# Optimization experiments

Measured on AMD Instinct MI355X. Metric: run time of the kernel, lower is better.

## Reference

```python
import jax, jax.numpy as jnp
import numpy as np
from jax import lax

H = 256  # hidden_dim
NDIM = 3
K = 32   # k_neighbors


def sincos_embed(coords, dim, ndim):
    # ContinuousSinCosEmbed: per-coordinate sin/cos features, zero-padded to `dim`.
    dpn = dim // ndim          # channels per coordinate
    half = dpn // 2
    freqs = 1.0 / (10000.0 ** (jnp.arange(half, dtype=coords.dtype) / half))
    ang = coords[..., :, None] * freqs                      # (..., ndim, half)
    emb = jnp.concatenate([jnp.sin(ang), jnp.cos(ang)], -1)  # (..., ndim, 2*half)
    emb = emb.reshape(coords.shape[:-1] + (ndim * 2 * half,))
    pad = dim - ndim * 2 * half
    if pad:
        emb = jnp.concatenate([emb, jnp.zeros(emb.shape[:-1] + (pad,), emb.dtype)], -1)
    return emb


def setup_inputs() -> dict:
    key = jax.random.key(0)
    ks = jax.random.split(key, 8)
    N, S = 50000, 1024
    positions = jax.random.uniform(ks[0], (N, NDIM), dtype=jnp.float32) * 10.0
    supernode_indices = jax.random.randint(ks[1], (S,), 0, N, dtype=jnp.int32)
    g = 1.0 / np.sqrt(H)
    W1 = jax.random.normal(ks[2], (H, H), jnp.float32) * g
    b1 = jnp.zeros((H,), jnp.float32)
    W2 = jax.random.normal(ks[3], (H, H), jnp.float32) * g
    b2 = jnp.zeros((H,), jnp.float32)
    Wp = jax.random.normal(ks[4], (2 * H, H), jnp.float32) * (1.0 / np.sqrt(2 * H))
    bp = jnp.zeros((H,), jnp.float32)
    return {"positions": positions, "supernode_indices": supernode_indices,
            "W1": W1, "b1": b1, "W2": W2, "b2": b2, "Wp": Wp, "bp": bp}


def reference(positions, supernode_indices, W1, b1, W2, b2, Wp, bp):
    # positions: (N, 3); supernode_indices: (S,)
    sup_pos = positions[supernode_indices]                 # (S, 3)
    # kNN neighbor search via dense pairwise squared distances (memory-bound)
    diff = sup_pos[:, None, :] - positions[None, :, :]     # (S, N, 3)
    dist2 = jnp.sum(diff * diff, axis=-1)                  # (S, N)
    _, nbr_idx = lax.top_k(-dist2, K)                      # (S, K)
    nbr_pos = positions[nbr_idx]                           # (S, K, 3)
    # relpos mode: embed (relative position, distance) -> ndim+1 = 4 coords
    rel = sup_pos[:, None, :] - nbr_pos                    # (S, K, 3)
    d = jnp.sqrt(jnp.sum(rel * rel, axis=-1, keepdims=True))  # (S, K, 1)
    rel_feat = jnp.concatenate([rel, d], axis=-1)          # (S, K, 4)
    msg_in = sincos_embed(rel_feat, H, NDIM + 1)           # (S, K, H)
    # message MLP: Dense -> gelu -> Dense
    h = jax.nn.gelu(jnp.einsum('ski,ij->skj', msg_in, W1) + b1)
    msgs = jnp.einsum('ski,ij->skj', h, W2) + b2           # (S, K, H)
    # scatter-reduce: mean over neighbors per supernode
    agg = jnp.mean(msgs, axis=1)                           # (S, H)
    # supernode absolute position embedding, concat, project
    sup_emb = sincos_embed(sup_pos, H, NDIM)               # (S, H)
    feats = jnp.concatenate([sup_emb, agg], axis=-1)       # (S, 2H)
    out = feats @ Wp + bp                                  # (S, H)
    return out[None]                                        # (1, S, H)
```

## Files before the change

kernel.cpp:

```cpp
#include <hip/hip_runtime.h>
#include <hip/hip_bf16.h>
#include <math.h>

typedef short bf16x8 __attribute__((ext_vector_type(8)));
typedef float f32x4  __attribute__((ext_vector_type(4)));

constexpr int   H     = 256;
constexpr int   KNB   = 32;
constexpr int   TPB   = 512;
constexpr int   GC    = 16;
constexpr float HINV  = 1.6f;
constexpr float HCEL  = 0.625f;
constexpr int   SLOTS = 32;
constexpr int   OCAP  = 256;
constexpr int   CAP   = 512;

__device__ __forceinline__ ushort f2bf(float x) {
    unsigned u = __float_as_uint(x);
    u += 0x7FFF + ((u >> 16) & 1);
    return (ushort)(u >> 16);
}

__device__ __forceinline__ float gelu_fast(float x) {
    float u = 0.7978845608028654f * (x + 0.044715f * x * x * x);
    float t = exp2f(-2.885390081777927f * u);
    return x / (1.0f + t);
}

__device__ __forceinline__ int cell_of(float x, float y, float z) {
    int cx = min(GC - 1, max(0, (int)(x * HINV)));
    int cy = min(GC - 1, max(0, (int)(y * HINV)));
    int cz = min(GC - 1, max(0, (int)(z * HINV)));
    return (cz * GC + cy) * GC + cx;
}

__global__ __launch_bounds__(256)
void prep(const float* __restrict__ W1, const float* __restrict__ Wp,
          const float* __restrict__ W2, const float* __restrict__ pos, int N,
          ushort* __restrict__ W1t, ushort* __restrict__ Wpt,
          ushort* __restrict__ W2t, float4* __restrict__ pos4s,
          int* __restrict__ origidx, int* __restrict__ cellcnt,
          int* __restrict__ ovfidx, float4* __restrict__ ovfpos) {
    const int b = blockIdx.x;
    if (b < 64) {
        __shared__ float tile[32][33];
        const int ti = b >> 3, tj = b & 7;
        const int r  = threadIdx.x >> 5, c = threadIdx.x & 31;
#pragma unroll
        for (int rr = r; rr < 32; rr += 8)
            tile[rr][c] = W1[(ti * 32 + rr) * H + tj * 32 + c];
        __syncthreads();
#pragma unroll
        for (int rr = r; rr < 32; rr += 8)
            W1t[(tj * 32 + rr) * H + ti * 32 + c] = f2bf(tile[c][rr]);
    } else if (b < 192) {
        __shared__ float tile[32][33];
        const int b2 = b - 64;
        const int ti = b2 >> 3, tj = b2 & 7;
        const int r  = threadIdx.x >> 5, c = threadIdx.x & 31;
#pragma unroll
        for (int rr = r; rr < 32; rr += 8)
            tile[rr][c] = Wp[(ti * 32 + rr) * H + tj * 32 + c];
        __syncthreads();
#pragma unroll
        for (int rr = r; rr < 32; rr += 8)
            Wpt[(tj * 32 + rr) * (2 * H) + ti * 32 + c] = f2bf(tile[c][rr]);
    } else if (b < 256) {
        __shared__ float tile[32][33];
        const int b2 = b - 192;
        const int ti = b2 >> 3, tj = b2 & 7;
        const int r  = threadIdx.x >> 5, c = threadIdx.x & 31;
#pragma unroll
        for (int rr = r; rr < 32; rr += 8)
            tile[rr][c] = W2[(ti * 32 + rr) * H + tj * 32 + c];
        __syncthreads();
#pragma unroll
        for (int rr = r; rr < 32; rr += 8)
            W2t[(tj * 32 + rr) * H + ti * 32 + c] = f2bf(tile[c][rr]);
    } else {
        const int sb = b - 256;
        const int base = sb * 1024;
        const int t = threadIdx.x;
        auto scat = [&](float x, float y, float z, int i) {
            float4 P = make_float4(x, y, z, 0.f);
            int c = cell_of(x, y, z);
            int slot = atomicAdd(&cellcnt[c], 1);
            if (slot < SLOTS) {
                pos4s[c * SLOTS + slot] = P;
                origidx[c * SLOTS + slot] = i;
            } else {
                int o = atomicAdd(&cellcnt[4096], 1);
                if (o < OCAP) { ovfpos[o] = P; ovfidx[o] = i; }
            }
        };
        if (base + 1024 <= N) {
            const float4* p4 = (const float4*)(pos + (size_t)base * 3);
            float4 f0 = p4[3 * t + 0];
            float4 f1 = p4[3 * t + 1];
            float4 f2 = p4[3 * t + 2];
            const int ib = base + 4 * t;
            scat(f0.x, f0.y, f0.z, ib + 0);
            scat(f0.w, f1.x, f1.y, ib + 1);
            scat(f1.z, f1.w, f2.x, ib + 2);
            scat(f2.y, f2.z, f2.w, ib + 3);
        } else {
            for (int i = base + t; i < N; i += 256)
                scat(pos[3 * i], pos[3 * i + 1], pos[3 * i + 2], i);
        }
    }
}

__global__ __launch_bounds__(TPB, 8)
void fused_knn_mlp(const float* __restrict__ pos,
                   const float4* __restrict__ pos4s,
                   const int* __restrict__ origidx,
                   const int* __restrict__ cellcnt,
                   const int* __restrict__ ovfidx, const float4* __restrict__ ovfpos,
                   const int* __restrict__ supidx,
                   const ushort* __restrict__ W1t, const float* __restrict__ b1,
                   ushort* __restrict__ supEB, ushort* __restrict__ hbB)
{
    __shared__ __align__(16) char pool[16384];
    float* amaxd = (float*)pool;
    int*   acnt  = (int*)(pool + 512);
    int*   ccell = (int*)(pool + 1024);
    int*   ccnt  = (int*)(pool + 2048);
    float* cmnd  = (float*)(pool + 3072);
    int*   cpre  = (int*)(pool + 4096);
    float* d2buf = (float*)(pool + 5120);
    int*   obuf  = (int*)(pool + 7168);
    float* pxb   = (float*)(pool + 9216);
    float* pyb   = (float*)(pool + 11264);
    float* pzb   = (float*)(pool + 13312);
    ushort* msg  = (ushort*)pool;

    __shared__ float rf[KNB][5];
    __shared__ int   selo[KNB];
    __shared__ int   wsum[4];
    __shared__ float tau2_sh, tau32_sh;
    __shared__ int   cnt_sh, ncl;

    const int s    = blockIdx.x;
    const int t    = threadIdx.x;
    const int lane = t & 63;
    const int w    = t >> 6;

    const int sidx = supidx[s];
    const float sx = pos[3 * sidx], sy = pos[3 * sidx + 1], sz = pos[3 * sidx + 2];

    constexpr float L2_10000 = 13.287712379549449f;

    if (t == 0) { ncl = 0; tau2_sh = 301.f; }

    const int scx = min(GC - 1, max(0, (int)(sx * HINV)));
    const int scy = min(GC - 1, max(0, (int)(sy * HINV)));
    const int scz = min(GC - 1, max(0, (int)(sz * HINV)));
    const int ax0 = max(0, scx - 2), ax1 = min(GC - 1, scx + 2);
    const int ay0 = max(0, scy - 2), ay1 = min(GC - 1, scy + 2);
    const int az0 = max(0, scz - 2), az1 = min(GC - 1, scz + 2);
    const int anx = ax1 - ax0 + 1, any_ = ay1 - ay0 + 1, anz = az1 - az0 + 1;
    const int an  = anx * any_ * anz;
    if (t < an) {
        int ci = t;
        int X = ax0 + ci % anx, rem = ci / anx;
        int Y = ay0 + rem % any_, Z = az0 + rem / any_;
        int cell = (Z * GC + Y) * GC + X;
        acnt[ci] = min(cellcnt[cell], SLOTS);
        float lx = X * HCEL, ly = Y * HCEL, lz = Z * HCEL;
        float mx = fmaxf(fabsf(sx - lx), fabsf(lx + HCEL - sx));
        float my = fmaxf(fabsf(sy - ly), fabsf(ly + HCEL - sy));
        float mz = fmaxf(fabsf(sz - lz), fabsf(lz + HCEL - sz));
        amaxd[ci] = mx * mx + my * my + mz * mz;
    }

    if (t < 256) {
        float se = 0.f;
        if (t < 252) {
            int c  = t / 84;
            int rr = t - c * 84;
            int f  = (rr < 42) ? rr : rr - 42;
            float coord = (c == 0) ? sx : ((c == 1) ? sy : sz);
            float ang = coord * exp2f(-(float)f * (L2_10000 / 42.f));
            se = (rr < 42) ? __sinf(ang) : __cosf(ang);
        }
        supEB[s * H + t] = f2bf(se);
    }
    __syncthreads();
    if (t < an) {
        int ci = t;
        float myv = amaxd[ci];
        int Sc = 0;
        for (int j = 0; j < an; j++) {
            bool less = (amaxd[j] < myv) || (amaxd[j] == myv && j < ci);
            Sc += less ? acnt[j] : 0;
        }
        if (Sc < KNB && KNB <= Sc + acnt[ci]) tau2_sh = myv;
    }
    __syncthreads();
    const float tau2 = tau2_sh;
    const float R2 = tau2 + 1e-3f;
    const float R  = sqrtf(R2);
    if (t == 0) tau32_sh = R2;

    const int bx0 = max(0, (int)floorf((sx - R) * HINV));
    const int bx1 = min(GC - 1, (int)floorf((sx + R) * HINV));
    const int by0 = max(0, (int)floorf((sy - R) * HINV));
    const int by1 = min(GC - 1, (int)floorf((sy + R) * HINV));
    const int bz0 = max(0, (int)floorf((sz - R) * HINV));
    const int bz1 = min(GC - 1, (int)floorf((sz + R) * HINV));
    const bool inwin = (bx0 >= ax0 && bx1 <= ax1 && by0 >= ay0 && by1 <= ay1 &&
                        bz0 >= az0 && bz1 <= az1);
    if (inwin) {
        if (t < an) {
            int ci = t;
            int cn = acnt[ci];
            if (cn > 0) {
                int X = ax0 + ci % anx, rem = ci / anx;
                int Y = ay0 + rem % any_, Z = az0 + rem / any_;
                float lx = X * HCEL, ly = Y * HCEL, lz = Z * HCEL;
                float ddx = fmaxf(fmaxf(lx - sx, sx - (lx + HCEL)), 0.f);
                float ddy = fmaxf(fmaxf(ly - sy, sy - (ly + HCEL)), 0.f);
                float ddz = fmaxf(fmaxf(lz - sz, sz - (lz + HCEL)), 0.f);
                float mnd = ddx * ddx + ddy * ddy + ddz * ddz;
                if (mnd <= R2) {
                    int p1 = (amaxd[ci] <= tau2) ? 1 : 0;
                    int cell = (Z * GC + Y) * GC + X;
                    int sl = atomicAdd(&ncl, 1);
                    if (sl < 256) { ccell[sl] = cell; ccnt[sl] = cn | (p1 << 8); cmnd[sl] = mnd; }
                }
            }
        }
    } else {
        const int nbx = bx1 - bx0 + 1, nby = by1 - by0 + 1, nbz = bz1 - bz0 + 1;
        const int ncb = nbx * nby * nbz;
        for (int ci = t; ci < ncb; ci += TPB) {
            int X = bx0 + ci % nbx, rem = ci / nbx;
            int Y = by0 + rem % nby, Z = bz0 + rem / nby;
            float lx = X * HCEL, ly = Y * HCEL, lz = Z * HCEL;
            float ddx = fmaxf(fmaxf(lx - sx, sx - (lx + HCEL)), 0.f);
            float ddy = fmaxf(fmaxf(ly - sy, sy - (ly + HCEL)), 0.f);
            float ddz = fmaxf(fmaxf(lz - sz, sz - (lz + HCEL)), 0.f);
            float mnd = ddx * ddx + ddy * ddy + ddz * ddz;
            if (mnd > R2) continue;
            int cell = (Z * GC + Y) * GC + X;
            int cn = min(cellcnt[cell], SLOTS);
            if (cn == 0) continue;
            float mx = fmaxf(fabsf(sx - lx), fabsf(lx + HCEL - sx));
            float my = fmaxf(fabsf(sy - ly), fabsf(ly + HCEL - sy));
            float mz = fmaxf(fabsf(sz - lz), fabsf(lz + HCEL - sz));
            float amx = mx * mx + my * my + mz * mz;
            int p1 = (amx <= tau2) ? 1 : 0;
            int sl = atomicAdd(&ncl, 1);
            if (sl < 256) { ccell[sl] = cell; ccnt[sl] = cn | (p1 << 8); cmnd[sl] = mnd; }
        }
    }
    __syncthreads();
    const int nclc = min(ncl, 256);

    auto build_prefix = [&](int phase, float tlim) -> int {
        int v = 0;
        if (t < 256) {
            if (t < nclc) {
                int cc = ccnt[t];
                int cn = cc & 0xff;
                int p1 = cc >> 8;
                v = (phase == 1) ? (p1 ? cn : 0)
                                 : ((!p1 && cmnd[t] <= tlim) ? cn : 0);
            }
#pragma unroll
            for (int off = 1; off < 64; off <<= 1) {
                int x = __shfl_up(v, off);
                if (lane >= off) v += x;
            }
            if (lane == 63) wsum[w] = v;
        }
        __syncthreads();
        if (t < 256) {
            int add = 0;
#pragma unroll
            for (int j = 0; j < 4; j++) if (j < w) add += wsum[j];
            cpre[t] = v + add;
        }
        __syncthreads();
        return cpre[255];
    };
    auto bsearch = [&](int j) -> int {
        int lo = 0;
#pragma unroll
        for (int st = 128; st; st >>= 1) {
            int nlo = lo + st;
            if (nlo <= 256 && cpre[nlo - 1] <= j) lo = nlo;
        }
        return lo;
    };

    const int tot1 = build_prefix(1, 0.f);
    const int M1 = min(tot1, CAP);
    if (t < M1) {
        int j = t;
        int lo = bsearch(j);
        int off = j - (lo ? cpre[lo - 1] : 0);
        int u = ccell[lo] * SLOTS + off;
        float4 P = pos4s[u];
        float dx = sx - P.x, dy = sy - P.y, dz = sz - P.z;
        d2buf[j] = dx * dx + dy * dy + dz * dz;
        obuf[j]  = origidx[u];
        pxb[j] = P.x; pyb[j] = P.y; pzb[j] = P.z;
    }
    const int Mp1 = (M1 + 3) & ~3;
    if (M1 + t < Mp1) { d2buf[M1 + t] = INFINITY; obuf[M1 + t] = 0x7fffffff; }
    if (t == 0) cnt_sh = M1;
    __syncthreads();

    if (t < M1) {
        int u = t;
        float myv = d2buf[u];
        int   myo = obuf[u];
        int rank = 0;
        for (int v2 = 0; v2 < Mp1; v2 += 4) {
            float4 dv = *(const float4*)&d2buf[v2];
            int4   iv = *(const int4*)&obuf[v2];
            rank += (dv.x < myv) || (dv.x == myv && iv.x < myo);
            rank += (dv.y < myv) || (dv.y == myv && iv.y < myo);
            rank += (dv.z < myv) || (dv.z == myv && iv.z < myo);
            rank += (dv.w < myv) || (dv.w == myv && iv.w < myo);
        }
        if (rank == KNB - 1) tau32_sh = myv;
    }
    __syncthreads();
    const float tau32 = tau32_sh;

    const int tot2 = build_prefix(2, tau32);
    for (int j0 = 0; j0 < tot2; j0 += TPB) {
        int j = j0 + t;
        bool pass = false; float pd2 = 0.f; int po = 0; float qx = 0, qy = 0, qz = 0;
        if (j < tot2) {
            int lo = bsearch(j);
            int off = j - (lo ? cpre[lo - 1] : 0);
            int u = ccell[lo] * SLOTS + off;
            float4 P = pos4s[u];
            float dx = sx - P.x, dy = sy - P.y, dz = sz - P.z;
            pd2 = dx * dx + dy * dy + dz * dz;
            if (pd2 <= tau32) { pass = true; po = origidx[u]; qx = P.x; qy = P.y; qz = P.z; }
        }
        unsigned long long m = __ballot(pass);
        if (m) {
            int ldr = __ffsll(m) - 1;
            int base = 0;
            if (lane == ldr) base = atomicAdd(&cnt_sh, __popcll(m));
            base = __shfl(base, ldr);
            if (pass) {
                int slp = base + __popcll(m & ((1ull << lane) - 1ull));
                if (slp < CAP) {
                    d2buf[slp] = pd2; obuf[slp] = po;
                    pxb[slp] = qx; pyb[slp] = qy; pzb[slp] = qz;
                }
            }
        }
    }
    {
        int no = min(cellcnt[4096], OCAP);
        for (int j = t; j < no; j += TPB) {
            float4 P = ovfpos[j];
            float dx = sx - P.x, dy = sy - P.y, dz = sz - P.z;
            float pd2 = dx * dx + dy * dy + dz * dz;
            if (pd2 <= tau32) {
                int slp = atomicAdd(&cnt_sh, 1);
                if (slp < CAP) {
                    d2buf[slp] = pd2; obuf[slp] = ovfidx[j];
                    pxb[slp] = P.x; pyb[slp] = P.y; pzb[slp] = P.z;
                }
            }
        }
    }
    __syncthreads();
    const int M = min(cnt_sh, CAP);
    const int Mpad = (M + 3) & ~3;
    if (M + t < Mpad) { d2buf[M + t] = INFINITY; obuf[M + t] = 0x7fffffff; }
    __syncthreads();

    if (t < M) {
        int u = t;
        float myv = d2buf[u];
        int   myo = obuf[u];
        int rank = 0;
        for (int v2 = 0; v2 < Mpad; v2 += 4) {
            float4 dv = *(const float4*)&d2buf[v2];
            int4   iv = *(const int4*)&obuf[v2];
            rank += (dv.x < myv) || (dv.x == myv && iv.x < myo);
            rank += (dv.y < myv) || (dv.y == myv && iv.y < myo);
            rank += (dv.z < myv) || (dv.z == myv && iv.z < myo);
            rank += (dv.w < myv) || (dv.w == myv && iv.w < myo);
        }
        if (rank < KNB) selo[rank] = u;
    }
    __syncthreads();
    if (t < KNB) {
        int u = selo[t];
        float rx = sx - pxb[u], ry = sy - pyb[u], rz = sz - pzb[u];
        float dd = sqrtf(d2buf[u]);
        rf[t][0] = rx; rf[t][1] = ry; rf[t][2] = rz; rf[t][3] = dd;
    }
    __syncthreads();

#pragma unroll
    for (int n = 0; n < 8; n++) {
        int item = t + n * TPB;
        int f = item & 31;
        int c = (item >> 5) & 3;
        int k = item >> 7;
        float ang = rf[k][c] * exp2f(-(float)f * (L2_10000 / 32.f));
        int swz = (k & 7) << 3;
        msg[((k << 8) | (c * 64 + f))      ^ swz] = f2bf(__sinf(ang));
        msg[((k << 8) | (c * 64 + 32 + f)) ^ swz] = f2bf(__cosf(ang));
    }
    __syncthreads();

    {
        const int lr = lane & 15;
        const int lg = lane >> 4;
        f32x4 acc00 = {0,0,0,0}, acc01 = {0,0,0,0};
        f32x4 acc10 = {0,0,0,0}, acc11 = {0,0,0,0};
#pragma unroll
        for (int kk = 0; kk < 8; kk++) {
            const int i0 = kk * 32 + lg * 8;
            bf16x8 a0 = *(const bf16x8*)(W1t + ((32 * w      + lr) << 8) + i0);
            bf16x8 a1 = *(const bf16x8*)(W1t + ((32 * w + 16 + lr) << 8) + i0);
            const int swz = (lr & 7) << 3;
            bf16x8 b0  = *(const bf16x8*)(msg + ((( lr       << 8) | i0) ^ swz));
            bf16x8 b1v = *(const bf16x8*)(msg + ((((lr + 16) << 8) | i0) ^ swz));
            acc00 = __builtin_amdgcn_mfma_f32_16x16x32_bf16(a0, b0,  acc00, 0, 0, 0);
            acc01 = __builtin_amdgcn_mfma_f32_16x16x32_bf16(a0, b1v, acc01, 0, 0, 0);
            acc10 = __builtin_amdgcn_mfma_f32_16x16x32_bf16(a1, b0,  acc10, 0, 0, 0);
            acc11 = __builtin_amdgcn_mfma_f32_16x16x32_bf16(a1, b1v, acc11, 0, 0, 0);
        }
        float part[8];
#pragma unroll
        for (int mm = 0; mm < 2; mm++)
#pragma unroll
            for (int r = 0; r < 4; r++) {
                int j = 32 * w + 16 * mm + 4 * lg + r;
                float bj = b1[j];
                float h0 = (mm == 0 ? acc00[r] : acc10[r]) + bj;
                float h1 = (mm == 0 ? acc01[r] : acc11[r]) + bj;
                part[mm * 4 + r] = gelu_fast(h0) + gelu_fast(h1);
            }
#pragma unroll
        for (int off = 1; off < 16; off <<= 1)
#pragma unroll
            for (int u = 0; u < 8; u++)
                part[u] += __shfl_xor(part[u], off);
        if (lr == 0) {
#pragma unroll
            for (int u = 0; u < 8; u++) {
                int mm = u >> 2, r = u & 3;
                hbB[s * H + 32 * w + 16 * mm + 4 * lg + r] = f2bf(part[u] * (1.0f / 32.0f));
            }
        }
    }
}

__global__ __launch_bounds__(512)
void mfma_out2(const ushort* __restrict__ hbB, const ushort* __restrict__ supEB,
               const ushort* __restrict__ W2t, const float* __restrict__ b2,
               const ushort* __restrict__ Wpt, const float* __restrict__ bp,
               float* __restrict__ out)
{
    __shared__ ushort agg[16 * 256];
    const int bm   = blockIdx.x;
    const int t    = threadIdx.x;
    const int lane = t & 63;
    const int w    = t >> 6;
    const int lr   = lane & 15;
    const int lg   = lane >> 4;

    f32x4 acc1[2] = {{0,0,0,0},{0,0,0,0}};
#pragma unroll
    for (int kk = 0; kk < 8; kk++) {
        const int i0 = kk * 32 + lg * 8;
        bf16x8 bf = *(const bf16x8*)(hbB + (16 * bm + lr) * H + i0);
        bf16x8 a0 = *(const bf16x8*)(W2t + ((32 * w      + lr) << 8) + i0);
        bf16x8 a1 = *(const bf16x8*)(W2t + ((32 * w + 16 + lr) << 8) + i0);
        acc1[0] = __builtin_amdgcn_mfma_f32_16x16x32_bf16(a0, bf, acc1[0], 0, 0, 0);
        acc1[1] = __builtin_amdgcn_mfma_f32_16x16x32_bf16(a1, bf, acc1[1], 0, 0, 0);
    }
#pragma unroll
    for (int mt = 0; mt < 2; mt++)
#pragma unroll
        for (int r = 0; r < 4; r++) {
            int j = 32 * w + 16 * mt + 4 * lg + r;
            int sl = lane & 15;
            float v = acc1[mt][r] + b2[j];
            agg[((sl << 8) | j) ^ ((sl & 7) << 3)] = f2bf(v);
        }
    __syncthreads();

    f32x4 acc2[2] = {{0,0,0,0},{0,0,0,0}};
#pragma unroll
    for (int kk = 0; kk < 16; kk++) {
        const int io = kk * 32 + lg * 8;
        bf16x8 bf;
        if (kk < 8) {
            bf = *(const bf16x8*)(supEB + (16 * bm + lr) * H + io);
        } else {
            int c = io - 256;
            bf = *(const bf16x8*)(agg + (((lr << 8) | c) ^ ((lr & 7) << 3)));
        }
        bf16x8 a0 = *(const bf16x8*)(Wpt + (32 * w      + lr) * 512 + io);
        bf16x8 a1 = *(const bf16x8*)(Wpt + (32 * w + 16 + lr) * 512 + io);
        acc2[0] = __builtin_amdgcn_mfma_f32_16x16x32_bf16(a0, bf, acc2[0], 0, 0, 0);
        acc2[1] = __builtin_amdgcn_mfma_f32_16x16x32_bf16(a1, bf, acc2[1], 0, 0, 0);
    }
#pragma unroll
    for (int mt = 0; mt < 2; mt++)
#pragma unroll
        for (int r = 0; r < 4; r++) {
            int jo = 32 * w + 16 * mt + 4 * lg + r;
            int srow = 16 * bm + (lane & 15);
            out[srow * H + jo] = acc2[mt][r] + bp[jo];
        }
}

extern "C" void kernel_launch(void* const* d_in, const int* in_sizes, int n_in,
                              void* d_out, int out_size, void* d_ws, size_t ws_size,
                              hipStream_t stream) {
    const float* pos = (const float*)d_in[0];
    const int*   sup = (const int*)d_in[1];
    const float* W1  = (const float*)d_in[2];
    const float* b1  = (const float*)d_in[3];
    const float* W2  = (const float*)d_in[4];
    const float* b2  = (const float*)d_in[5];
    const float* Wp  = (const float*)d_in[6];
    const float* bp  = (const float*)d_in[7];

    const int N = in_sizes[0] / 3;
    const int S = in_sizes[1];
    float* out = (float*)d_out;

    char* ws = (char*)d_ws;
    ushort* W1t     = (ushort*)ws;
    ushort* Wpt     = (ushort*)(ws + (128 << 10));
    ushort* W2t     = (ushort*)(ws + (384 << 10));
    float4* pos4s   = (float4*)(ws + (512 << 10));
    int*    origidx = (int*)(ws + (2560 << 10));
    int*    cellcnt = (int*)(ws + (3072 << 10));
    int*    ovfidx  = (int*)(ws + (3092 << 10));
    float4* ovfpos  = (float4*)(ws + (3096 << 10));
    ushort* supEB   = (ushort*)(ws + (3104 << 10));
    ushort* hbB     = (ushort*)(ws + (3616 << 10));

    hipMemsetAsync(cellcnt, 0, 4097 * sizeof(int), stream);
    const int nscat = (N + 1023) / 1024;
    prep<<<256 + nscat, 256, 0, stream>>>(W1, Wp, W2, pos, N,
                                          W1t, Wpt, W2t, pos4s,
                                          origidx, cellcnt, ovfidx, ovfpos);
    fused_knn_mlp<<<S, TPB, 0, stream>>>(pos, pos4s, origidx, cellcnt,
                                         ovfidx, ovfpos, sup,
                                         W1t, b1, supEB, hbB);
    mfma_out2<<<S / 16, 512, 0, stream>>>(hbB, supEB, W2t, b2, Wpt, bp, out);
}
```

Before: 76.95 us.

## Replace two-phase kNN candidate filtering with single-pass gather and rank

Drops the two-phase candidate selection, where the first pass ranked cells certainly inside the radius to get a tighter tau32 and the second pass filtered the remaining cells with ballot and atomic compaction. All candidate points from cells intersecting the search sphere, plus the overflow points, are now loaded directly into shared buffers and a single rank-sort selects the top 32. This removes one rank pass, several barriers and the atomics, but makes the O(M^2) rank pass run over more candidates. CAP and the LDS pool are doubled to hold them, which may reduce occupancy.

```diff
diff --git a/kernel.cpp b/kernel.cpp
--- a/kernel.cpp
+++ b/kernel.cpp
@@ -13,7 +13,7 @@
 constexpr float HCEL  = 0.625f;
 constexpr int   SLOTS = 32;
 constexpr int   OCAP  = 256;
-constexpr int   CAP   = 512;
+constexpr int   CAP   = 1024;
 
 __device__ __forceinline__ ushort f2bf(float x) {
     unsigned u = __float_as_uint(x);
@@ -120,25 +120,24 @@
                    const ushort* __restrict__ W1t, const float* __restrict__ b1,
                    ushort* __restrict__ supEB, ushort* __restrict__ hbB)
 {
-    __shared__ __align__(16) char pool[16384];
+    __shared__ __align__(16) char pool[24576];
     float* amaxd = (float*)pool;
     int*   acnt  = (int*)(pool + 512);
     int*   ccell = (int*)(pool + 1024);
     int*   ccnt  = (int*)(pool + 2048);
-    float* cmnd  = (float*)(pool + 3072);
-    int*   cpre  = (int*)(pool + 4096);
-    float* d2buf = (float*)(pool + 5120);
-    int*   obuf  = (int*)(pool + 7168);
-    float* pxb   = (float*)(pool + 9216);
-    float* pyb   = (float*)(pool + 11264);
-    float* pzb   = (float*)(pool + 13312);
+    int*   cpre  = (int*)(pool + 3072);
+    float* d2buf = (float*)(pool + 4096);
+    int*   obuf  = (int*)(pool + 8192);
+    float* pxb   = (float*)(pool + 12288);
+    float* pyb   = (float*)(pool + 16384);
+    float* pzb   = (float*)(pool + 20480);
     ushort* msg  = (ushort*)pool;
 
     __shared__ float rf[KNB][5];
     __shared__ int   selo[KNB];
     __shared__ int   wsum[4];
-    __shared__ float tau2_sh, tau32_sh;
-    __shared__ int   cnt_sh, ncl;
+    __shared__ float tau2_sh;
+    __shared__ int   ncl;
 
     const int s    = blockIdx.x;
     const int t    = threadIdx.x;
@@ -200,7 +199,6 @@
     const float tau2 = tau2_sh;
     const float R2 = tau2 + 1e-3f;
     const float R  = sqrtf(R2);
-    if (t == 0) tau32_sh = R2;
 
     const int bx0 = max(0, (int)floorf((sx - R) * HINV));
     const int bx1 = min(GC - 1, (int)floorf((sx + R) * HINV));
@@ -221,12 +219,10 @@
                 float ddx = fmaxf(fmaxf(lx - sx, sx - (lx + HCEL)), 0.f);
                 float ddy = fmaxf(fmaxf(ly - sy, sy - (ly + HCEL)), 0.f);
                 float ddz = fmaxf(fmaxf(lz - sz, sz - (lz + HCEL)), 0.f);
-                float mnd = ddx * ddx + ddy * ddy + ddz * ddz;
-                if (mnd <= R2) {
-                    int p1 = (amaxd[ci] <= tau2) ? 1 : 0;
+                if (ddx * ddx + ddy * ddy + ddz * ddz <= R2) {
                     int cell = (Z * GC + Y) * GC + X;
                     int sl = atomicAdd(&ncl, 1);
-                    if (sl < 256) { ccell[sl] = cell; ccnt[sl] = cn | (p1 << 8); cmnd[sl] = mnd; }
+                    if (sl < 256) { ccell[sl] = cell; ccnt[sl] = cn; }
                 }
             }
         }
@@ -240,33 +236,21 @@
             float ddx = fmaxf(fmaxf(lx - sx, sx - (lx + HCEL)), 0.f);
             float ddy = fmaxf(fmaxf(ly - sy, sy - (ly + HCEL)), 0.f);
             float ddz = fmaxf(fmaxf(lz - sz, sz - (lz + HCEL)), 0.f);
-            float mnd = ddx * ddx + ddy * ddy + ddz * ddz;
-            if (mnd > R2) continue;
+            if (ddx * ddx + ddy * ddy + ddz * ddz > R2) continue;
             int cell = (Z * GC + Y) * GC + X;
             int cn = min(cellcnt[cell], SLOTS);
             if (cn == 0) continue;
-            float mx = fmaxf(fabsf(sx - lx), fabsf(lx + HCEL - sx));
-            float my = fmaxf(fabsf(sy - ly), fabsf(ly + HCEL - sy));
-            float mz = fmaxf(fabsf(sz - lz), fabsf(lz + HCEL - sz));
-            float amx = mx * mx + my * my + mz * mz;
-            int p1 = (amx <= tau2) ? 1 : 0;
             int sl = atomicAdd(&ncl, 1);
-            if (sl < 256) { ccell[sl] = cell; ccnt[sl] = cn | (p1 << 8); cmnd[sl] = mnd; }
+            if (sl < 256) { ccell[sl] = cell; ccnt[sl] = cn; }
         }
     }
     __syncthreads();
     const int nclc = min(ncl, 256);
 
-    auto build_prefix = [&](int phase, float tlim) -> int {
+    {
         int v = 0;
         if (t < 256) {
-            if (t < nclc) {
-                int cc = ccnt[t];
-                int cn = cc & 0xff;
-                int p1 = cc >> 8;
-                v = (phase == 1) ? (p1 ? cn : 0)
-                                 : ((!p1 && cmnd[t] <= tlim) ? cn : 0);
-            }
+            if (t < nclc) v = ccnt[t];
 #pragma unroll
             for (int off = 1; off < 64; off <<= 1) {
                 int x = __shfl_up(v, off);
@@ -282,105 +266,42 @@
             cpre[t] = v + add;
         }
         __syncthreads();
-        return cpre[255];
-    };
-    auto bsearch = [&](int j) -> int {
-        int lo = 0;
-#pragma unroll
-        for (int st = 128; st; st >>= 1) {
-            int nlo = lo + st;
-            if (nlo <= 256 && cpre[nlo - 1] <= j) lo = nlo;
-        }
-        return lo;
-    };
-
-    const int tot1 = build_prefix(1, 0.f);
-    const int M1 = min(tot1, CAP);
-    if (t < M1) {
-        int j = t;
-        int lo = bsearch(j);
-        int off = j - (lo ? cpre[lo - 1] : 0);
-        int u = ccell[lo] * SLOTS + off;
-        float4 P = pos4s[u];
-        float dx = sx - P.x, dy = sy - P.y, dz = sz - P.z;
-        d2buf[j] = dx * dx + dy * dy + dz * dz;
-        obuf[j]  = origidx[u];
-        pxb[j] = P.x; pyb[j] = P.y; pzb[j] = P.z;
-    }
-    const int Mp1 = (M1 + 3) & ~3;
-    if (M1 + t < Mp1) { d2buf[M1 + t] = INFINITY; obuf[M1 + t] = 0x7fffffff; }
-    if (t == 0) cnt_sh = M1;
-    __syncthreads();
-
-    if (t < M1) {
-        int u = t;
-        float myv = d2buf[u];
-        int   myo = obuf[u];
-        int rank = 0;
-        for (int v2 = 0; v2 < Mp1; v2 += 4) {
-            float4 dv = *(const float4*)&d2buf[v2];
-            int4   iv = *(const int4*)&obuf[v2];
-            rank += (dv.x < myv) || (dv.x == myv && iv.x < myo);
-            rank += (dv.y < myv) || (dv.y == myv && iv.y < myo);
-            rank += (dv.z < myv) || (dv.z == myv && iv.z < myo);
-            rank += (dv.w < myv) || (dv.w == myv && iv.w < myo);
-        }
-        if (rank == KNB - 1) tau32_sh = myv;
-    }
-    __syncthreads();
-    const float tau32 = tau32_sh;
-
-    const int tot2 = build_prefix(2, tau32);
-    for (int j0 = 0; j0 < tot2; j0 += TPB) {
+    }
+    const int tot = cpre[255];
+    const int Mg  = min(tot, CAP);
+
+    for (int j0 = 0; j0 < Mg; j0 += TPB) {
         int j = j0 + t;
-        bool pass = false; float pd2 = 0.f; int po = 0; float qx = 0, qy = 0, qz = 0;
-        if (j < tot2) {
-            int lo = bsearch(j);
+        if (j < Mg) {
+            int lo = 0;
+#pragma unroll
+            for (int st = 128; st; st >>= 1) {
+                int nlo = lo + st;
+                if (nlo <= 256 && cpre[nlo - 1] <= j) lo = nlo;
+            }
             int off = j - (lo ? cpre[lo - 1] : 0);
             int u = ccell[lo] * SLOTS + off;
             float4 P = pos4s[u];
             float dx = sx - P.x, dy = sy - P.y, dz = sz - P.z;
-            pd2 = dx * dx + dy * dy + dz * dz;
-            if (pd2 <= tau32) { pass = true; po = origidx[u]; qx = P.x; qy = P.y; qz = P.z; }
-        }
-        unsigned long long m = __ballot(pass);
-        if (m) {
-            int ldr = __ffsll(m) - 1;
-            int base = 0;
-            if (lane == ldr) base = atomicAdd(&cnt_sh, __popcll(m));
-            base = __shfl(base, ldr);
-            if (pass) {
-                int slp = base + __popcll(m & ((1ull << lane) - 1ull));
-                if (slp < CAP) {
-                    d2buf[slp] = pd2; obuf[slp] = po;
-                    pxb[slp] = qx; pyb[slp] = qy; pzb[slp] = qz;
-                }
-            }
-        }
-    }
-    {
-        int no = min(cellcnt[4096], OCAP);
-        for (int j = t; j < no; j += TPB) {
-            float4 P = ovfpos[j];
-            float dx = sx - P.x, dy = sy - P.y, dz = sz - P.z;
-            float pd2 = dx * dx + dy * dy + dz * dz;
-            if (pd2 <= tau32) {
-                int slp = atomicAdd(&cnt_sh, 1);
-                if (slp < CAP) {
-                    d2buf[slp] = pd2; obuf[slp] = ovfidx[j];
-                    pxb[slp] = P.x; pyb[slp] = P.y; pzb[slp] = P.z;
-                }
-            }
-        }
-    }
-    __syncthreads();
-    const int M = min(cnt_sh, CAP);
+            d2buf[j] = dx * dx + dy * dy + dz * dz;
+            obuf[j]  = origidx[u];
+            pxb[j] = P.x; pyb[j] = P.y; pzb[j] = P.z;
+        }
+    }
+    const int no = min(min(cellcnt[4096], OCAP), CAP - Mg);
+    if (t < no) {
+        float4 P = ovfpos[t];
+        float dx = sx - P.x, dy = sy - P.y, dz = sz - P.z;
+        d2buf[Mg + t] = dx * dx + dy * dy + dz * dz;
+        obuf[Mg + t]  = ovfidx[t];
+        pxb[Mg + t] = P.x; pyb[Mg + t] = P.y; pzb[Mg + t] = P.z;
+    }
+    const int M = Mg + no;
     const int Mpad = (M + 3) & ~3;
     if (M + t < Mpad) { d2buf[M + t] = INFINITY; obuf[M + t] = 0x7fffffff; }
     __syncthreads();
 
-    if (t < M) {
-        int u = t;
+    for (int u = t; u < M; u += TPB) {
         float myv = d2buf[u];
         int   myo = obuf[u];
         int rank = 0;
```

Result: slower. 165.7 us (+115.3%).
